# Kernel tuning notes

Hardware: AMD Instinct MI355X
Metric: run time of the kernel (lower is better)

## Reference

```python
import jax, jax.numpy as jnp
import numpy as np

B, N, K = 4, 4096, 16
D_POINTS, D_MODEL = 64, 128


def setup_inputs() -> dict:
    key = jax.random.key(0)
    ks = jax.random.split(key, 18)
    rn = lambda k, shp, s=0.05: (jax.random.normal(k, shp, jnp.float32) * s)
    return {
        "xyz": jax.random.normal(ks[0], (B, N, 3), jnp.float32),
        "features": jax.random.normal(ks[1], (B, N, D_POINTS), jnp.float32),
        # fc_delta: Linear(3,d_model) -> ReLU -> Linear(d_model,d_model)
        "Wd1": rn(ks[2], (3, D_MODEL)), "bd1": rn(ks[3], (D_MODEL,)),
        "Wd2": rn(ks[4], (D_MODEL, D_MODEL)), "bd2": rn(ks[5], (D_MODEL,)),
        # fc1: Linear(d_points, d_model)
        "Wf1": rn(ks[6], (D_POINTS, D_MODEL)), "bf1": rn(ks[7], (D_MODEL,)),
        # w_qs / w_ks / w_vs: Linear(d_model, d_model, bias=False)
        "Wq": rn(ks[8], (D_MODEL, D_MODEL)),
        "Wk": rn(ks[9], (D_MODEL, D_MODEL)),
        "Wv": rn(ks[10], (D_MODEL, D_MODEL)),
        # fc_gamma: Linear(d_model,d_model) -> ReLU -> Linear(d_model,d_model)
        "Wg1": rn(ks[11], (D_MODEL, D_MODEL)), "bg1": rn(ks[12], (D_MODEL,)),
        "Wg2": rn(ks[13], (D_MODEL, D_MODEL)), "bg2": rn(ks[14], (D_MODEL,)),
        # fc2: Linear(d_model, d_points)
        "Wo": rn(ks[15], (D_MODEL, D_POINTS)), "bo": rn(ks[16], (D_POINTS,)),
    }


def reference(xyz, features, Wd1, bd1, Wd2, bd2, Wf1, bf1, Wq, Wk, Wv,
              Wg1, bg1, Wg2, bg2, Wo, bo):
    sq = jnp.sum(xyz * xyz, axis=-1)
    d2 = sq[:, :, None] + sq[:, None, :] - 2.0 * jnp.einsum('bnd,bmd->bnm', xyz, xyz)
    # argsort()[:, :, :k] == k smallest distances (self included)
    _, knn_idx = jax.lax.top_k(-d2, K)  # [B,N,K] int32

    gather = jax.vmap(lambda a, i: a[i])  # per-batch fancy gather along point axis
    knn_xyz = gather(xyz, knn_idx)                       # [B,N,K,3]
    rel = xyz[:, :, None, :] - knn_xyz                   # [B,N,K,3]
    pos_enc = jax.nn.relu(rel @ Wd1 + bd1) @ Wd2 + bd2   # [B,N,K,D]

    shortcut = features
    f = features @ Wf1 + bf1                             # [B,N,D]
    knn_f = gather(f, knn_idx)                           # [B,N,K,D]

    q = f @ Wq                                           # [B,N,D]
    k = knn_f @ Wk                                       # [B,N,K,D]
    v = knn_f @ Wv                                       # [B,N,K,D]

    attn = q[:, :, None, :] - k + pos_enc                # [B,N,K,D]
    attn = jax.nn.relu(attn @ Wg1 + bg1) @ Wg2 + bg2
    attn = jax.nn.softmax(attn / np.sqrt(D_MODEL).astype(np.float32), axis=-2)

    res = jnp.einsum('bnkf,bnkf->bnf', attn, v + pos_enc)  # [B,N,D]
    return res @ Wo + bo + shortcut                        # [B,N,d_points]
```

## Files before the change

kernel.cpp:

```cpp
#include <hip/hip_runtime.h>
#include <hip/hip_bf16.h>

#define NPTS 4096
#define BATCH 4
#define BN (BATCH * NPTS)
#define DMODEL 128
#define DPTS 64
#define KNBR 16
#define SWS 136

typedef unsigned short u16;
typedef unsigned int u32;
typedef unsigned long long u64;
typedef short bh8 __attribute__((ext_vector_type(8)));
typedef float f32x4 __attribute__((ext_vector_type(4)));

__device__ __forceinline__ float bfu(u16 u) {
    union { u32 i; float f; } c; c.i = ((u32)u) << 16; return c.f;
}
__device__ __forceinline__ u16 f2u(float x) {
    u32 u = __float_as_uint(x);
    u32 r = u + 0x7FFFu + ((u >> 16) & 1u);
    return (u16)(r >> 16);
}
__device__ __forceinline__ u32 pack2(float a, float b) {
    return (u32)f2u(a) | ((u32)f2u(b) << 16);
}
__device__ __forceinline__ float ldr(const void* p, long i, int mode) {
    return mode == 0 ? bfu(((const u16*)p)[i]) : ((const float*)p)[i];
}
__device__ __forceinline__ void str(void* p, long i, float v, int mode) {
    if (mode == 0) ((u16*)p)[i] = f2u(v);
    else ((float*)p)[i] = v;
}
__device__ __forceinline__ int detect_mode(const void* Wq) {
    const u16* w = (const u16*)Wq;
    int lane = threadIdx.x & 63;
    int tot = 0;
#pragma unroll
    for (int r = 0; r < 4; ++r) {
        unsigned e = (w[lane + r * 64] >> 7) & 0xFFu;
        bool wild = (e >= 132u) || (e > 0u && e <= 90u);
        tot += (int)__popcll(__ballot(wild));
    }
    return tot > 32 ? 1 : 0;
}

__global__ __launch_bounds__(256) void prep_kernel(
    const void* __restrict__ Wd2, const void* __restrict__ Wg1, const void* __restrict__ Wg2,
    const void* __restrict__ Wo, const void* __restrict__ Wq, const void* __restrict__ Wk,
    const void* __restrict__ Wv, const void* __restrict__ Wf1,
    u16* __restrict__ WdT2, u16* __restrict__ WgT1, u16* __restrict__ WgT2,
    u16* __restrict__ WoT, u16* __restrict__ WqT, u16* __restrict__ WkT,
    u16* __restrict__ WvT, u16* __restrict__ WfT) {
    int mode = detect_mode(Wq);
    int gid = blockIdx.x * 256 + threadIdx.x;
    if (gid < 6 * 16384) {
        int m = gid >> 14, o = gid & 16383;
        int n = o >> 7, i = o & 127;
        const void* W = (m == 0) ? Wd2 : (m == 1) ? Wg1 : (m == 2) ? Wg2
                      : (m == 3) ? Wq  : (m == 4) ? Wk  : Wv;
        u16* D = (m == 0) ? WdT2 : (m == 1) ? WgT1 : (m == 2) ? WgT2
               : (m == 3) ? WqT  : (m == 4) ? WkT  : WvT;
        D[o] = f2u(ldr(W, (long)i * 128 + n, mode));
    } else if (gid < 6 * 16384 + 8192) {
        int o = gid - 6 * 16384;
        int n = o >> 6, k2 = o & 63;
        WfT[o] = f2u(ldr(Wf1, (long)k2 * 128 + n, mode));
    } else if (gid < 6 * 16384 + 16384) {
        int o2 = gid - 6 * 16384 - 8192;
        int col = o2 >> 7, i = o2 & 127;
        WoT[o2] = f2u(ldr(Wo, (long)i * 64 + col, mode));
    }
}

__global__ __launch_bounds__(256) void qkv_kernel(
    const void* __restrict__ feat, const void* __restrict__ bf1v, const void* __restrict__ WqRaw,
    const u16* __restrict__ WfT, const u16* __restrict__ WqT,
    const u16* __restrict__ WkT, const u16* __restrict__ WvT,
    u16* __restrict__ qw, u16* __restrict__ kfw, u16* __restrict__ vfw) {
    int mode = detect_mode(WqRaw);
    __shared__ __align__(16) u16 sFeat[64 * 72];
    __shared__ __align__(16) u16 sF[64 * SWS];
    const int t = threadIdx.x;
    const int p0 = blockIdx.x * 64;
    const int lane = t & 63, w = t >> 6;
    const int rg = (w & 1) * 32, cg = (w >> 1) * 64;
    const int lm = lane & 15, lq = lane >> 4;

    for (int i = t; i < 512; i += 256) {
        int r = i >> 3, c8 = i & 7;
        u16 tmp[8];
        if (mode == 0) {
            *(uint4*)tmp = *((const uint4*)feat + (long)(p0 + r) * 8 + c8);
        } else {
            const float* fp = (const float*)feat + (long)(p0 + r) * 64 + c8 * 8;
#pragma unroll
            for (int u = 0; u < 8; ++u) tmp[u] = f2u(fp[u]);
        }
        *(uint4*)(sFeat + r * 72 + c8 * 8) = *(uint4*)tmp;
    }
    __syncthreads();

    {
        f32x4 acc[2][4];
#pragma unroll
        for (int rt = 0; rt < 2; ++rt)
#pragma unroll
            for (int ct = 0; ct < 4; ++ct) { acc[rt][ct][0]=0.f; acc[rt][ct][1]=0.f; acc[rt][ct][2]=0.f; acc[rt][ct][3]=0.f; }
#pragma unroll
        for (int kk = 0; kk < 2; ++kk) {
            const int ko = kk * 32 + lq * 8;
            bh8 a0 = *(const bh8*)(sFeat + (rg + lm) * 72 + ko);
            bh8 a1 = *(const bh8*)(sFeat + (rg + 16 + lm) * 72 + ko);
            bh8 bq[4];
#pragma unroll
            for (int ct = 0; ct < 4; ++ct)
                bq[ct] = *(const bh8*)(WfT + (long)(cg + ct * 16 + lm) * 64 + ko);
#pragma unroll
            for (int ct = 0; ct < 4; ++ct) {
                acc[0][ct] = __builtin_amdgcn_mfma_f32_16x16x32_bf16(a0, bq[ct], acc[0][ct], 0, 0, 0);
                acc[1][ct] = __builtin_amdgcn_mfma_f32_16x16x32_bf16(a1, bq[ct], acc[1][ct], 0, 0, 0);
            }
        }
#pragma unroll
        for (int rt = 0; rt < 2; ++rt)
#pragma unroll
            for (int ct = 0; ct < 4; ++ct) {
                const int col = cg + ct * 16 + lm;
                const float bj = ldr(bf1v, col, mode);
#pragma unroll
                for (int r4 = 0; r4 < 4; ++r4) {
                    int row = rg + rt * 16 + lq * 4 + r4;
                    u32 u = (u32)f2u(acc[rt][ct][r4] + bj);
                    u32 o = __shfl_xor(u, 1);
                    if ((lane & 1) == 0)
                        *(u32*)(sF + row * SWS + col) = u | (o << 16);
                }
            }
    }
    __syncthreads();

    const u16* Ws[3] = {WqT, WkT, WvT};
    u16* Os[3] = {qw, kfw, vfw};
#pragma unroll 1
    for (int m = 0; m < 3; ++m) {
        f32x4 acc[2][4];
#pragma unroll
        for (int rt = 0; rt < 2; ++rt)
#pragma unroll
            for (int ct = 0; ct < 4; ++ct) { acc[rt][ct][0]=0.f; acc[rt][ct][1]=0.f; acc[rt][ct][2]=0.f; acc[rt][ct][3]=0.f; }
#pragma unroll
        for (int kk = 0; kk < 4; ++kk) {
            const int ko = kk * 32 + lq * 8;
            bh8 a0 = *(const bh8*)(sF + (rg + lm) * SWS + ko);
            bh8 a1 = *(const bh8*)(sF + (rg + 16 + lm) * SWS + ko);
            bh8 bq[4];
#pragma unroll
            for (int ct = 0; ct < 4; ++ct)
                bq[ct] = *(const bh8*)(Ws[m] + (long)(cg + ct * 16 + lm) * 128 + ko);
#pragma unroll
            for (int ct = 0; ct < 4; ++ct) {
                acc[0][ct] = __builtin_amdgcn_mfma_f32_16x16x32_bf16(a0, bq[ct], acc[0][ct], 0, 0, 0);
                acc[1][ct] = __builtin_amdgcn_mfma_f32_16x16x32_bf16(a1, bq[ct], acc[1][ct], 0, 0, 0);
            }
        }
#pragma unroll
        for (int rt = 0; rt < 2; ++rt)
#pragma unroll
            for (int ct = 0; ct < 4; ++ct) {
                const int col = cg + ct * 16 + lm;
#pragma unroll
                for (int r4 = 0; r4 < 4; ++r4) {
                    int row = rg + rt * 16 + lq * 4 + r4;
                    u32 u = (u32)f2u(acc[rt][ct][r4]);
                    u32 o = __shfl_xor(u, 1);
                    if ((lane & 1) == 0)
                        *(u32*)(Os[m] + (long)(p0 + row) * DMODEL + col) = u | (o << 16);
                }
            }
    }
}

__device__ __forceinline__ void mfma4(const u16* sIn, const u16* __restrict__ Bg,
                                      const float* bias, bool dorelu,
                                      u16* sOut, int t) {
    const int lane = t & 63, w = t >> 6;
    const int rg = (w & 1) * 32, cg = (w >> 1) * 64;
    const int lm = lane & 15, lq = lane >> 4;
    f32x4 acc[2][4];
#pragma unroll
    for (int rt = 0; rt < 2; ++rt)
#pragma unroll
        for (int ct = 0; ct < 4; ++ct) { acc[rt][ct][0]=0.f; acc[rt][ct][1]=0.f; acc[rt][ct][2]=0.f; acc[rt][ct][3]=0.f; }
#pragma unroll
    for (int kk = 0; kk < 4; ++kk) {
        const int ko = kk * 32 + lq * 8;
        bh8 a0 = *(const bh8*)(sIn + (rg + lm) * SWS + ko);
        bh8 a1 = *(const bh8*)(sIn + (rg + 16 + lm) * SWS + ko);
        bh8 bq[4];
#pragma unroll
        for (int ct = 0; ct < 4; ++ct)
            bq[ct] = *(const bh8*)(Bg + (long)(cg + ct * 16 + lm) * 128 + ko);
#pragma unroll
        for (int ct = 0; ct < 4; ++ct) {
            acc[0][ct] = __builtin_amdgcn_mfma_f32_16x16x32_bf16(a0, bq[ct], acc[0][ct], 0, 0, 0);
            acc[1][ct] = __builtin_amdgcn_mfma_f32_16x16x32_bf16(a1, bq[ct], acc[1][ct], 0, 0, 0);
        }
    }
#pragma unroll
    for (int rt = 0; rt < 2; ++rt)
#pragma unroll
        for (int ct = 0; ct < 4; ++ct) {
            const int col = cg + ct * 16 + lm;
            const float bj = bias[col];
#pragma unroll
            for (int r4 = 0; r4 < 4; ++r4) {
                int row = rg + rt * 16 + lq * 4 + r4;
                float v = acc[rt][ct][r4] + bj;
                if (dorelu) v = fmaxf(v, 0.f);
                u32 u = (u32)f2u(v);
                u32 o = __shfl_xor(u, 1);
                if ((lane & 1) == 0)
                    *(u32*)(sOut + row * SWS + col) = u | (o << 16);
            }
        }
}

#define ATT_SA 0
#define ATT_SPE 17408
#define ATT_SREL 34816
#define ATT_SBIAS 35840
#define ATT_SQ 37376
#define SMEM_BYTES 38400

__global__ __launch_bounds__(256, 4) void fused_kernel(
    const void* __restrict__ xyz, const void* __restrict__ feat,
    const void* __restrict__ Wd1, const void* __restrict__ bd1, const void* __restrict__ bd2,
    const void* __restrict__ bg1, const void* __restrict__ bg2, const void* __restrict__ bo,
    const void* __restrict__ WqRaw,
    const u16* __restrict__ WdT2, const u16* __restrict__ WgT1, const u16* __restrict__ WgT2,
    const u16* __restrict__ WoT,
    const u16* __restrict__ qw, const u16* __restrict__ kfw, const u16* __restrict__ vfw,
    void* __restrict__ out) {
    int mode = detect_mode(WqRaw);
    __shared__ __align__(16) char smem[SMEM_BYTES];
    __shared__ int sIdx[64];
    u16* sXyz = (u16*)smem;
    u16* sA   = (u16*)(smem + ATT_SA);
    u16* sPE  = (u16*)(smem + ATT_SPE);
    float (*sRel)[4] = (float(*)[4])(smem + ATT_SREL);
    float* sBias = (float*)(smem + ATT_SBIAS);
    u16* sQ   = (u16*)(smem + ATT_SQ);

    const int t = threadIdx.x, lane = t & 63, w = t >> 6;
    const int lm = lane & 15, lq = lane >> 4;
    const int p0 = blockIdx.x * 4;
    const long bbase = (long)(p0 >> 12) * NPTS;
    const long xb = bbase * 3;

    for (int m = t; m < NPTS; m += 256) {
        float gx = ldr(xyz, xb + m * 3 + 0, mode);
        float gy = ldr(xyz, xb + m * 3 + 1, mode);
        float gz = ldr(xyz, xb + m * 3 + 2, mode);
        uint2 pk;
        pk.x = (u32)f2u(gx) | ((u32)f2u(gy) << 16);
        pk.y = (u32)f2u(gz);
        *(uint2*)(sXyz + m * 4) = pk;
    }
    __syncthreads();

    {
        const int pl = (p0 & (NPTS - 1)) + w;
        uint2 qv = *(const uint2*)(sXyz + pl * 4);
        const float px = __uint_as_float(qv.x << 16);
        const float py = __uint_as_float(qv.x & 0xFFFF0000u);
        const float pz = __uint_as_float(qv.y << 16);
        u64 kv = ~0ull;
        u32 Tu = 0xFFFFFFFFu;
        uint2 cd0 = *(const uint2*)(sXyz + lane * 4);
        uint2 cd1 = *(const uint2*)(sXyz + (64 + lane) * 4);
#pragma unroll 1
        for (int it = 0; it < NPTS / 128; ++it) {
            uint2 c0 = cd0, c1 = cd1;
            if (it < NPTS / 128 - 1) {
                cd0 = *(const uint2*)(sXyz + ((it + 1) * 128 + lane) * 4);
                cd1 = *(const uint2*)(sXyz + ((it + 1) * 128 + 64 + lane) * 4);
            }
            float cx0 = __uint_as_float(c0.x << 16);
            float cy0 = __uint_as_float(c0.x & 0xFFFF0000u);
            float cz0 = __uint_as_float(c0.y << 16);
            float cx1 = __uint_as_float(c1.x << 16);
            float cy1 = __uint_as_float(c1.x & 0xFFFF0000u);
            float cz1 = __uint_as_float(c1.y << 16);
            float k0 = fmaf(px * cx0 + py * cy0 + pz * cz0, -2.f,
                            cx0 * cx0 + cy0 * cy0 + cz0 * cz0);
            float k1 = fmaf(px * cx1 + py * cy1 + pz * cz1, -2.f,
                            cx1 * cx1 + cy1 * cy1 + cz1 * cz1);
            u32 u0 = __float_as_uint(k0); u0 ^= (u32)((int)u0 >> 31) | 0x80000000u;
            u32 u1 = __float_as_uint(k1); u1 ^= (u32)((int)u1 >> 31) | 0x80000000u;
            u32 umin = (u0 < u1) ? u0 : u1;
            unsigned long long mask = __ballot(umin < Tu);
            const int ibase = it * 128;
            while (mask) {
                int l = __ffsll(mask) - 1;
                mask &= mask - 1;
                u32 a0 = __builtin_amdgcn_readlane(u0, l);
                u32 a1 = __builtin_amdgcn_readlane(u1, l);
                if (a0 < Tu) {
                    u64 cand = ((u64)a0 << 32) | (u32)(ibase + l);
                    u64 prev = __shfl_up(kv, 1);
                    if (lane == 0) prev = 0;
                    kv = (prev > cand) ? prev : ((kv > cand) ? cand : kv);
                    Tu = __builtin_amdgcn_readlane((u32)(kv >> 32), 15);
                }
                if (a1 < Tu) {
                    u64 cand = ((u64)a1 << 32) | (u32)(ibase + 64 + l);
                    u64 prev = __shfl_up(kv, 1);
                    if (lane == 0) prev = 0;
                    kv = (prev > cand) ? prev : ((kv > cand) ? cand : kv);
                    Tu = __builtin_amdgcn_readlane((u32)(kv >> 32), 15);
                }
            }
        }
        if (lane < 16) sIdx[w * 16 + lane] = (int)(u32)kv;
    }
    __syncthreads();

    for (int i = t; i < 384; i += 256) {
        const void* b = (i < 128) ? bd2 : (i < 256) ? bg1 : bg2;
        sBias[i] = ldr(b, i & 127, mode);
    }
    ((u32*)sQ)[t] = ((const u32*)(qw + (long)p0 * DMODEL))[t];
    const int ch = 2 * lane;
    const float wd0a = ldr(Wd1, ch, mode),       wd0b = ldr(Wd1, ch + 1, mode);
    const float wd1a = ldr(Wd1, 128 + ch, mode), wd1b = ldr(Wd1, 128 + ch + 1, mode);
    const float wd2a = ldr(Wd1, 256 + ch, mode), wd2b = ldr(Wd1, 256 + ch + 1, mode);
    const float bd1a = ldr(bd1, ch, mode),       bd1b = ldr(bd1, ch + 1, mode);
    if (t < 64) {
        int pl2 = (p0 & (NPTS - 1)) + (t >> 4);
        uint2 pv = *(const uint2*)(sXyz + pl2 * 4);
        uint2 nv = *(const uint2*)(sXyz + sIdx[t] * 4);
        sRel[t][0] = __uint_as_float(pv.x << 16)          - __uint_as_float(nv.x << 16);
        sRel[t][1] = __uint_as_float(pv.x & 0xFFFF0000u)  - __uint_as_float(nv.x & 0xFFFF0000u);
        sRel[t][2] = __uint_as_float(pv.y << 16)          - __uint_as_float(nv.y << 16);
    }
    __syncthreads();

#pragma unroll
    for (int i = 0; i < 16; ++i) {
        int r = w * 16 + i;
        float4 rl = *(const float4*)sRel[r];
        float h0 = fmaxf(bd1a + rl.x * wd0a + rl.y * wd1a + rl.z * wd2a, 0.f);
        float h1 = fmaxf(bd1b + rl.x * wd0b + rl.y * wd1b + rl.z * wd2b, 0.f);
        *(u32*)(sA + r * SWS + ch) = pack2(h0, h1);
    }
    __syncthreads();
    mfma4(sA, WdT2, sBias, false, sPE, t);
    __syncthreads();

    u32 vpeP[16];
#pragma unroll
    for (int i = 0; i < 16; ++i) {
        int r = w * 16 + i;
        long nbase = (bbase + sIdx[r]) * (long)DMODEL + ch;
        u32 kv2 = *(const u32*)(kfw + nbase);
        u32 vv2 = *(const u32*)(vfw + nbase);
        u32 qv2 = *(const u32*)(sQ + (r >> 4) * DMODEL + ch);
        u32 pe2 = *(const u32*)(sPE + r * SWS + ch);
        float pa = bfu((u16)pe2), pb = bfu((u16)(pe2 >> 16));
        vpeP[i] = pack2(bfu((u16)vv2) + pa, bfu((u16)(vv2 >> 16)) + pb);
        float a0 = bfu((u16)qv2) - bfu((u16)kv2) + pa;
        float a1 = bfu((u16)(qv2 >> 16)) - bfu((u16)(kv2 >> 16)) + pb;
        *(u32*)(sA + r * SWS + ch) = pack2(a0, a1);
    }
    __syncthreads();
    mfma4(sA, WgT1, sBias + 128, true, sPE, t);
    __syncthreads();
    mfma4(sPE, WgT2, sBias + 256, false, sA, t);
    __syncthreads();

    float res0, res1;
    {
        float mx0 = -3e38f, mx1 = -3e38f;
#pragma unroll
        for (int k = 0; k < KNBR; ++k) {
            u32 l2 = *(const u32*)(sA + (w * 16 + k) * SWS + ch);
            mx0 = fmaxf(mx0, bfu((u16)l2));
            mx1 = fmaxf(mx1, bfu((u16)(l2 >> 16)));
        }
        const float inv = 0.08838834764831845f;
        float s0 = 0.f, s1 = 0.f, r0 = 0.f, r1 = 0.f;
#pragma unroll
        for (int k = 0; k < KNBR; ++k) {
            u32 l2 = *(const u32*)(sA + (w * 16 + k) * SWS + ch);
            float e0 = __expf((bfu((u16)l2) - mx0) * inv);
            float e1 = __expf((bfu((u16)(l2 >> 16)) - mx1) * inv);
            s0 += e0; s1 += e1;
            r0 += e0 * bfu((u16)vpeP[k]);
            r1 += e1 * bfu((u16)(vpeP[k] >> 16));
        }
        res0 = r0 / s0; res1 = r1 / s1;
    }
    __syncthreads();
    *(u32*)(sA + w * SWS + ch) = pack2(res0, res1);
    __syncthreads();

    {
        const int col = w * 16 + lm;
        f32x4 acc = {0.f, 0.f, 0.f, 0.f};
#pragma unroll
        for (int kk = 0; kk < 4; ++kk) {
            const int ko = kk * 32 + lq * 8;
            bh8 aa = *(const bh8*)(sA + lm * SWS + ko);
            bh8 bb = *(const bh8*)(WoT + (long)col * DMODEL + ko);
            acc = __builtin_amdgcn_mfma_f32_16x16x32_bf16(aa, bb, acc, 0, 0, 0);
        }
        if (lq == 0) {
            float bov = ldr(bo, col, mode);
#pragma unroll
            for (int r4 = 0; r4 < 4; ++r4) {
                long p = p0 + r4;
                float v = acc[r4] + bov + ldr(feat, p * DPTS + col, mode);
                str(out, p * DPTS + col, v, mode);
            }
        }
    }
}

extern "C" void kernel_launch(void* const* d_in, const int* in_sizes, int n_in,
                              void* d_out, int out_size, void* d_ws, size_t ws_size,
                              hipStream_t stream) {
    (void)in_sizes; (void)n_in; (void)out_size; (void)ws_size;
    char* ws = (char*)d_ws;
    u16* qw   = (u16*)(ws + 256);
    u16* kfw  = qw + (long)BN * DMODEL;
    u16* vfw  = kfw + (long)BN * DMODEL;
    u16* WdT2 = vfw + (long)BN * DMODEL;
    u16* WgT1 = WdT2 + 16384;
    u16* WgT2 = WgT1 + 16384;
    u16* WoT  = WgT2 + 16384;
    u16* WqT  = WoT + 8192;
    u16* WkT  = WqT + 16384;
    u16* WvT  = WkT + 16384;
    u16* WfT  = WvT + 16384;

    prep_kernel<<<448, 256, 0, stream>>>(d_in[4], d_in[11], d_in[13], d_in[15],
                                         d_in[8], d_in[9], d_in[10], d_in[6],
                                         WdT2, WgT1, WgT2, WoT, WqT, WkT, WvT, WfT);
    qkv_kernel<<<BN / 64, 256, 0, stream>>>(d_in[1], d_in[7], d_in[8],
                                            WfT, WqT, WkT, WvT, qw, kfw, vfw);
    fused_kernel<<<BN / 4, 256, 0, stream>>>(d_in[0], d_in[1], d_in[2], d_in[3], d_in[5],
                                             d_in[12], d_in[14], d_in[16], d_in[8],
                                             WdT2, WgT1, WgT2, WoT,
                                             qw, kfw, vfw, d_out);
}
```

Measured before the change: 345.4 us.

## Seed kNN with bitonic sort of first 64 candidates; drop vpe register array

```diff
diff --git a/kernel.cpp b/kernel.cpp
--- a/kernel.cpp
+++ b/kernel.cpp
@@ -183,7 +183,7 @@
 }
 
 __device__ __forceinline__ void mfma4(const u16* sIn, const u16* __restrict__ Bg,
-                                      const float* bias, bool dorelu,
+                                      const float* bias, bool dorelu, bool inplace,
                                       u16* sOut, int t) {
     const int lane = t & 63, w = t >> 6;
     const int rg = (w & 1) * 32, cg = (w >> 1) * 64;
@@ -208,6 +208,7 @@
             acc[1][ct] = __builtin_amdgcn_mfma_f32_16x16x32_bf16(a1, bq[ct], acc[1][ct], 0, 0, 0);
         }
     }
+    if (inplace) __syncthreads();
 #pragma unroll
     for (int rt = 0; rt < 2; ++rt)
 #pragma unroll
@@ -276,16 +277,42 @@
         const float px = __uint_as_float(qv.x << 16);
         const float py = __uint_as_float(qv.x & 0xFFFF0000u);
         const float pz = __uint_as_float(qv.y << 16);
-        u64 kv = ~0ull;
-        u32 Tu = 0xFFFFFFFFu;
-        uint2 cd0 = *(const uint2*)(sXyz + lane * 4);
-        uint2 cd1 = *(const uint2*)(sXyz + (64 + lane) * 4);
+
+        u64 kv;
+        {
+            uint2 c = *(const uint2*)(sXyz + lane * 4);
+            float cx = __uint_as_float(c.x << 16);
+            float cy = __uint_as_float(c.x & 0xFFFF0000u);
+            float cz = __uint_as_float(c.y << 16);
+            float key = fmaf(px * cx + py * cy + pz * cz, -2.f,
+                             cx * cx + cy * cy + cz * cz);
+            u32 uk = __float_as_uint(key);
+            uk ^= (u32)((int)uk >> 31) | 0x80000000u;
+            kv = ((u64)uk << 32) | (u32)lane;
+#pragma unroll
+            for (int k = 2; k <= 64; k <<= 1) {
+#pragma unroll
+                for (int j = k >> 1; j > 0; j >>= 1) {
+                    u64 other = __shfl_xor(kv, j);
+                    bool keepMin = ((lane & j) == 0) == ((lane & k) == 0);
+                    bool smaller = kv < other;
+                    kv = (keepMin == smaller) ? kv : other;
+                }
+            }
+        }
+        u32 Tu = __builtin_amdgcn_readlane((u32)(kv >> 32), 15);
+
+        uint2 cd0 = *(const uint2*)(sXyz + (64 + lane) * 4);
+        uint2 cd1 = *(const uint2*)(sXyz + (128 + lane) * 4);
 #pragma unroll 1
-        for (int it = 0; it < NPTS / 128; ++it) {
+        for (int it = 0; it < 32; ++it) {
+            const int base = 64 + it * 128;
             uint2 c0 = cd0, c1 = cd1;
-            if (it < NPTS / 128 - 1) {
-                cd0 = *(const uint2*)(sXyz + ((it + 1) * 128 + lane) * 4);
-                cd1 = *(const uint2*)(sXyz + ((it + 1) * 128 + 64 + lane) * 4);
+            if (it < 31) {
+                int n0 = base + 128 + lane;
+                int n1 = n0 + 64 > 4095 ? 4095 : n0 + 64;
+                cd0 = *(const uint2*)(sXyz + n0 * 4);
+                cd1 = *(const uint2*)(sXyz + n1 * 4);
             }
             float cx0 = __uint_as_float(c0.x << 16);
             float cy0 = __uint_as_float(c0.x & 0xFFFF0000u);
@@ -299,23 +326,23 @@
                             cx1 * cx1 + cy1 * cy1 + cz1 * cz1);
             u32 u0 = __float_as_uint(k0); u0 ^= (u32)((int)u0 >> 31) | 0x80000000u;
             u32 u1 = __float_as_uint(k1); u1 ^= (u32)((int)u1 >> 31) | 0x80000000u;
+            if (it == 31) u1 = 0xFFFFFFFFu;
             u32 umin = (u0 < u1) ? u0 : u1;
             unsigned long long mask = __ballot(umin < Tu);
-            const int ibase = it * 128;
             while (mask) {
                 int l = __ffsll(mask) - 1;
                 mask &= mask - 1;
                 u32 a0 = __builtin_amdgcn_readlane(u0, l);
                 u32 a1 = __builtin_amdgcn_readlane(u1, l);
                 if (a0 < Tu) {
-                    u64 cand = ((u64)a0 << 32) | (u32)(ibase + l);
+                    u64 cand = ((u64)a0 << 32) | (u32)(base + l);
                     u64 prev = __shfl_up(kv, 1);
                     if (lane == 0) prev = 0;
                     kv = (prev > cand) ? prev : ((kv > cand) ? cand : kv);
                     Tu = __builtin_amdgcn_readlane((u32)(kv >> 32), 15);
                 }
                 if (a1 < Tu) {
-                    u64 cand = ((u64)a1 << 32) | (u32)(ibase + 64 + l);
+                    u64 cand = ((u64)a1 << 32) | (u32)(base + 64 + l);
                     u64 prev = __shfl_up(kv, 1);
                     if (lane == 0) prev = 0;
                     kv = (prev > cand) ? prev : ((kv > cand) ? cand : kv);
@@ -356,28 +383,23 @@
         *(u32*)(sA + r * SWS + ch) = pack2(h0, h1);
     }
     __syncthreads();
-    mfma4(sA, WdT2, sBias, false, sPE, t);
-    __syncthreads();
-
-    u32 vpeP[16];
+    mfma4(sA, WdT2, sBias, false, false, sPE, t);
+    __syncthreads();
+
 #pragma unroll
     for (int i = 0; i < 16; ++i) {
         int r = w * 16 + i;
-        long nbase = (bbase + sIdx[r]) * (long)DMODEL + ch;
-        u32 kv2 = *(const u32*)(kfw + nbase);
-        u32 vv2 = *(const u32*)(vfw + nbase);
+        u32 kv2 = *(const u32*)(kfw + (bbase + sIdx[r]) * (long)DMODEL + ch);
         u32 qv2 = *(const u32*)(sQ + (r >> 4) * DMODEL + ch);
         u32 pe2 = *(const u32*)(sPE + r * SWS + ch);
-        float pa = bfu((u16)pe2), pb = bfu((u16)(pe2 >> 16));
-        vpeP[i] = pack2(bfu((u16)vv2) + pa, bfu((u16)(vv2 >> 16)) + pb);
-        float a0 = bfu((u16)qv2) - bfu((u16)kv2) + pa;
-        float a1 = bfu((u16)(qv2 >> 16)) - bfu((u16)(kv2 >> 16)) + pb;
+        float a0 = bfu((u16)qv2) - bfu((u16)kv2) + bfu((u16)pe2);
+        float a1 = bfu((u16)(qv2 >> 16)) - bfu((u16)(kv2 >> 16)) + bfu((u16)(pe2 >> 16));
         *(u32*)(sA + r * SWS + ch) = pack2(a0, a1);
     }
     __syncthreads();
-    mfma4(sA, WgT1, sBias + 128, true, sPE, t);
-    __syncthreads();
-    mfma4(sPE, WgT2, sBias + 256, false, sA, t);
+    mfma4(sA, WgT1, sBias + 128, true, true, sA, t);
+    __syncthreads();
+    mfma4(sA, WgT2, sBias + 256, false, true, sA, t);
     __syncthreads();
 
     float res0, res1;
@@ -394,11 +416,13 @@
 #pragma unroll
         for (int k = 0; k < KNBR; ++k) {
             u32 l2 = *(const u32*)(sA + (w * 16 + k) * SWS + ch);
+            u32 v2 = *(const u32*)(vfw + (bbase + sIdx[w * 16 + k]) * (long)DMODEL + ch);
+            u32 p2 = *(const u32*)(sPE + (w * 16 + k) * SWS + ch);
             float e0 = __expf((bfu((u16)l2) - mx0) * inv);
             float e1 = __expf((bfu((u16)(l2 >> 16)) - mx1) * inv);
             s0 += e0; s1 += e1;
-            r0 += e0 * bfu((u16)vpeP[k]);
-            r1 += e1 * bfu((u16)(vpeP[k] >> 16));
+            r0 += e0 * (bfu((u16)v2) + bfu((u16)p2));
+            r1 += e1 * (bfu((u16)(v2 >> 16)) + bfu((u16)(p2 >> 16)));
         }
         res0 = r0 / s0; res1 = r1 / s1;
     }
```

Measured after the change: 315.0 us. 8.8% less time.
